# Kernel optimization log

Measured on AMD Instinct MI355X. Metric: run time of the kernel, lower is better.

## Reference

```python
import jax, jax.numpy as jnp
import numpy as np

B, T, H, W, C = 8, 16, 64, 64, 16
HID = 64  # hidden_dim of each ConvLSTM cell
K = 3     # kernel size


def _convlstm_step(x, h, c, Wk, b):
    # conv over concat([x, h]) -> 4*HID gate channels (i, f, o, g)
    z = jax.lax.conv_general_dilated(
        jnp.concatenate([x, h], axis=-1), Wk,
        window_strides=(1, 1), padding='SAME',
        dimension_numbers=('NHWC', 'HWIO', 'NHWC')) + b
    i, f, o, g = jnp.split(z, 4, axis=-1)
    c_new = jax.nn.sigmoid(f) * c + jax.nn.sigmoid(i) * jnp.tanh(g)
    h_new = jax.nn.sigmoid(o) * jnp.tanh(c_new)
    return h_new, c_new


def setup_inputs() -> dict:
    key = jax.random.key(0)
    k1, k2, k3 = jax.random.split(key, 3)
    enc_input = jax.random.normal(k1, (B, T, H, W, C), jnp.float32)
    # input cell: in_channels = C + HID; stacked hidden cell: 2*HID
    W0 = jax.random.normal(k2, (K, K, C + HID, 4 * HID), jnp.float32) * 0.05
    b0 = jnp.zeros((4 * HID,), jnp.float32)
    W1 = jax.random.normal(k3, (K, K, 2 * HID, 4 * HID), jnp.float32) * 0.05
    b1 = jnp.zeros((4 * HID,), jnp.float32)
    return {"enc_input": enc_input, "W0": W0, "b0": b0, "W1": W1, "b1": b1}


def reference(enc_input, W0, b0, W1, b1):
    Bv, Tv, Hv, Wv, _ = enc_input.shape
    z0 = jnp.zeros((Bv, Hv, Wv, HID), enc_input.dtype)

    def step(carry, x_t):
        h0, c0, h1, c1 = carry
        h0, c0 = _convlstm_step(x_t, h0, c0, W0, b0)   # input ConvLSTM
        h1, c1 = _convlstm_step(h0, h1, c1, W1, b1)    # stacked hidden ConvLSTM
        return (h0, c0, h1, c1), None

    xs = jnp.moveaxis(enc_input, 1, 0)  # [T, B, H, W, C]
    (h0, c0, h1, c1), _ = jax.lax.scan(step, (z0, z0, z0, z0), xs)
    # Encoder returns last hidden layer's (h, c)
    return (h1, c1)
```

## Files before the change

### kernel.cpp

```cpp
#include <hip/hip_runtime.h>
#include <hip/hip_bf16.h>

#define Bv 8
#define Tv 16
#define Hv 64
#define Wv 64
#define Cv 16
#define HID 64
#define PH 66

typedef short short8 __attribute__((ext_vector_type(8)));
typedef float f32x4 __attribute__((ext_vector_type(4)));
typedef unsigned short u16x8 __attribute__((ext_vector_type(8)));

__device__ __forceinline__ unsigned short f2bf(float x) {
  union { float f; unsigned int u; } v; v.f = x;
  unsigned int r = v.u + 0x7FFF + ((v.u >> 16) & 1);
  return (unsigned short)(r >> 16);
}
__device__ __forceinline__ float sigmoid_f(float x) {
  return 1.f / (1.f + __expf(-x));
}
__device__ __forceinline__ float tanh_f(float x) {
  float e = __expf(2.f * x);
  return 1.f - 2.f / (e + 1.f);
}

__global__ void relayout_w1(const float* __restrict__ W1, unsigned short* __restrict__ out) {
  int o = blockIdx.x * 256 + threadIdx.x;
  if (o >= 36 * 8192) return;
  int cc = o >> 13, t = o & 8191;
  int wn = t >> 11, t2 = t & 2047;
  int g = t2 >> 9, t3 = t2 & 511;
  int l = t3 >> 3, e = t3 & 7;
  int kg = l >> 4, r = l & 15;
  int k = kg * 8 + e;
  int col = g * 64 + wn * 16 + r;
  int tap = cc >> 2, cgi = cc & 3;
  out[o] = f2bf(W1[(size_t)(tap * 128 + cgi * 32 + k) * 256 + col]);
}

__global__ void relayout_w0(const float* __restrict__ W0, unsigned short* __restrict__ out) {
  int o = blockIdx.x * 256 + threadIdx.x;
  if (o >= 23 * 8192) return;
  int cc = o >> 13, t = o & 8191;
  int wn = t >> 11, t2 = t & 2047;
  int g = t2 >> 9, t3 = t2 & 511;
  int l = t3 >> 3, e = t3 & 7;
  int kg = l >> 4, r = l & 15;
  int k = kg * 8 + e;
  int col = g * 64 + wn * 16 + r;
  float v = 0.f;
  if (cc < 4) {
    int tap = 2 * cc + (k >> 4);
    v = W0[(size_t)(tap * 80 + (k & 15)) * 256 + col];
  } else if (cc == 4) {
    if (k < 16) v = W0[(size_t)(8 * 80 + k) * 256 + col];
  } else {
    int hcc = cc - 5, tap = hcc >> 1, cgi = hcc & 1;
    v = W0[(size_t)(tap * 80 + 16 + cgi * 32 + k) * 256 + col];
  }
  out[o] = f2bf(v);
}

__global__ void zero_init(unsigned short* __restrict__ h0a, unsigned short* __restrict__ h0b,
                          unsigned short* __restrict__ h1a, unsigned short* __restrict__ h1b,
                          unsigned short* __restrict__ xb) {
  int idx = blockIdx.x * 256 + threadIdx.x;
  u16x8 z = {};
  const int XB_CH = (Bv * PH * PH * 16 * 2 * 2) / 16;
  if (idx < XB_CH) { *(u16x8*)(xb + idx * 8) = z; return; }
  idx -= XB_CH;
  int bufi = idx / 16640;
  if (bufi >= 4) return;
  int rem = idx - bufi * 16640;
  int b = rem / 2080, r2 = rem - b * 2080;
  int hp = r2 >> 3, c8 = r2 & 7;
  int y, x;
  if (hp < 66)       { y = 0;  x = hp; }
  else if (hp < 132) { y = 65; x = hp - 66; }
  else { int i2 = hp - 132; y = 1 + (i2 >> 1); x = (i2 & 1) * 65; }
  unsigned short* base = (bufi == 0) ? h0a : (bufi == 1) ? h0b : (bufi == 2) ? h1a : h1b;
  *(u16x8*)(base + ((size_t)((b * PH + y) * PH) + x) * 64 + c8 * 8) = z;
}

__global__ void convert_x0(const float* __restrict__ enc, unsigned short* __restrict__ xb) {
  int idx = blockIdx.x * 256 + threadIdx.x;
  int b = idx >> 12, pix = idx & 4095;
  int y = pix >> 6, x = pix & 63;
  const float* s = enc + ((size_t)(b * Tv + 0) * 4096 + pix) * 16;
  float4 f0 = *(const float4*)(s);
  float4 f1 = *(const float4*)(s + 4);
  float4 f2 = *(const float4*)(s + 8);
  float4 f3 = *(const float4*)(s + 12);
  u16x8 o0, o1;
  o0[0]=f2bf(f0.x); o0[1]=f2bf(f0.y); o0[2]=f2bf(f0.z); o0[3]=f2bf(f0.w);
  o0[4]=f2bf(f1.x); o0[5]=f2bf(f1.y); o0[6]=f2bf(f1.z); o0[7]=f2bf(f1.w);
  o1[0]=f2bf(f2.x); o1[1]=f2bf(f2.y); o1[2]=f2bf(f2.z); o1[3]=f2bf(f2.w);
  o1[4]=f2bf(f3.x); o1[5]=f2bf(f3.y); o1[6]=f2bf(f3.z); o1[7]=f2bf(f3.w);
  unsigned short* d = xb + ((size_t)((b * PH + y + 1) * PH) + (x + 1)) * 16;
  *(u16x8*)(d)     = o0;
  *(u16x8*)(d + 8) = o1;
}

template<int CELL, int NC>
__device__ __forceinline__ void cell_run(
    const char* __restrict__ A0, const char* __restrict__ A1,
    const char* __restrict__ Wr, const float* __restrict__ bias,
    float* __restrict__ cbuf, unsigned short* __restrict__ hout,
    float* __restrict__ h1fin, float* __restrict__ c1fin,
    char* lds, int b, int by, int bx, int tid)
{
  constexpr bool T0C = (CELL == 0) ? (NC == 5) : (NC == 18);
  const int l = tid & 63, w = tid >> 6;
  const int wm = w >> 2, wn = w & 3;
  const int r = l & 15, kg = l >> 4;
  const int j = wn * 16 + r;

  int pixs;
  {
    int ps = w * 16 + r;
    int ys = by * 16 + (ps >> 3), xs = bx * 8 + (ps & 7);
    pixs = (b * PH + ys) * PH + xs;
  }
  const int zpix = b * PH * PH;

  auto ISSUE = [&](int cc, int buf) {
    char* dst = lds + buf * 24576;
    if constexpr (CELL == 0) {
      if (cc < 5) {
        int tapA = 2 * cc;
        int kyA = tapA / 3, kxA = tapA - kyA * 3;
        unsigned offA = (unsigned)((pixs + kyA * PH + kxA) * 32 + kg * 16);
        unsigned offB;
        if (cc < 4) {
          int tapB = tapA + 1;
          int kyB = tapB / 3, kxB = tapB - kyB * 3;
          offB = (unsigned)((pixs + kyB * PH + kxB) * 32 + (kg - 2) * 16);
        } else {
          offB = (unsigned)(zpix * 32 + (kg - 2) * 16);
        }
        unsigned aoff = (kg < 2) ? offA : offB;
        __builtin_amdgcn_global_load_lds((const unsigned int*)(A0 + aoff),
                                         (unsigned int*)(dst + w * 1024), 16, 0, 0);
      } else {
        int hcc = cc - 5, tap = hcc >> 1, cgi = hcc & 1;
        int ky = tap / 3, kx = tap - ky * 3;
        unsigned aoff = (unsigned)((pixs + ky * PH + kx) * 128 + cgi * 64 + kg * 16);
        __builtin_amdgcn_global_load_lds((const unsigned int*)(A1 + aoff),
                                         (unsigned int*)(dst + w * 1024), 16, 0, 0);
      }
    } else {
      int tap, cgi;
      if (T0C) { tap = cc >> 1; cgi = cc & 1; }
      else     { tap = cc >> 2; cgi = cc & 3; }
      int ky = tap / 3, kx = tap - ky * 3;
      const char* srcb = (cgi < 2) ? A0 : A1;
      unsigned aoff = (unsigned)((pixs + ky * PH + kx) * 128 + (cgi & 1) * 64 + kg * 16);
      __builtin_amdgcn_global_load_lds((const unsigned int*)(srcb + aoff),
                                       (unsigned int*)(dst + w * 1024), 16, 0, 0);
    }
    int wcc;
    if constexpr (CELL == 0) wcc = cc;
    else                     wcc = T0C ? ((cc >> 1) * 4 + (cc & 1)) : cc;
    const char* wp = Wr + (size_t)wcc * 16384 + (unsigned)(w * 2048 + l * 16);
    __builtin_amdgcn_global_load_lds((const unsigned int*)(wp),
                                     (unsigned int*)(dst + 8192 + w * 2048), 16, 0, 0);
    __builtin_amdgcn_global_load_lds((const unsigned int*)(wp + 1024),
                                     (unsigned int*)(dst + 8192 + w * 2048 + 1024), 16, 0, 0);
  };

  f32x4 acc[4][4] = {};
  short8 af[4], bfv[4];

  ISSUE(0, 0); ISSUE(1, 1);
#pragma unroll
  for (int cc = 0; cc < NC; ++cc) {
    if (cc <= NC - 2) { asm volatile("s_waitcnt vmcnt(3)" ::: "memory"); }
    else              { asm volatile("s_waitcnt vmcnt(0)" ::: "memory"); }
    __builtin_amdgcn_sched_barrier(0);
    __builtin_amdgcn_s_barrier();
    __builtin_amdgcn_sched_barrier(0);

    if (cc + 2 < NC) ISSUE(cc + 2, (cc + 2) % 3);

    const char* bufp = lds + (cc % 3) * 24576;
#pragma unroll
    for (int mi = 0; mi < 4; ++mi)
      af[mi] = *(const short8*)(bufp + (wm * 4 + mi) * 1024 + l * 16);
#pragma unroll
    for (int g = 0; g < 4; ++g)
      bfv[g] = *(const short8*)(bufp + 8192 + (wn * 4 + g) * 1024 + l * 16);

#pragma unroll
    for (int mi = 0; mi < 4; ++mi)
#pragma unroll
      for (int g = 0; g < 4; ++g)
        acc[mi][g] = __builtin_amdgcn_mfma_f32_16x16x32_bf16(
            af[mi], bfv[g], acc[mi][g], 0, 0, 0);
  }

  float bi[4];
#pragma unroll
  for (int g = 0; g < 4; ++g) bi[g] = bias[g * 64 + j];
  float cpre[4][4];
#pragma unroll
  for (int mi = 0; mi < 4; ++mi) {
#pragma unroll
    for (int rg = 0; rg < 4; ++rg) {
      if constexpr (T0C) { cpre[mi][rg] = 0.f; }
      else {
        int p = wm * 64 + mi * 16 + kg * 4 + rg;
        int y = by * 16 + (p >> 3), x = bx * 8 + (p & 7);
        cpre[mi][rg] = cbuf[((size_t)((b * Hv + y) * Wv) + x) * HID + j];
      }
    }
  }
#pragma unroll
  for (int mi = 0; mi < 4; ++mi) {
#pragma unroll
    for (int rg = 0; rg < 4; ++rg) {
      int p = wm * 64 + mi * 16 + kg * 4 + rg;
      int y = by * 16 + (p >> 3), x = bx * 8 + (p & 7);
      float zi = acc[mi][0][rg] + bi[0];
      float zf = acc[mi][1][rg] + bi[1];
      float zo = acc[mi][2][rg] + bi[2];
      float zg = acc[mi][3][rg] + bi[3];
      float cn = sigmoid_f(zf) * cpre[mi][rg] + sigmoid_f(zi) * tanh_f(zg);
      float hn = sigmoid_f(zo) * tanh_f(cn);
      size_t ci = ((size_t)((b * Hv + y) * Wv) + x) * HID + j;
      cbuf[ci] = cn;
      hout[((size_t)((b * PH + y + 1) * PH) + (x + 1)) * HID + j] = f2bf(hn);
      if (CELL == 1 && h1fin != nullptr) {
        h1fin[ci] = hn;
        c1fin[ci] = cn;
      }
    }
  }
}

template<int NC1, int NC0, bool LAST>
__global__ __launch_bounds__(512, 4)
void step_fused(const unsigned short* __restrict__ xbr, unsigned short* __restrict__ xbw,
                const unsigned short* __restrict__ h0r, unsigned short* __restrict__ h0w,
                const unsigned short* __restrict__ h1r, unsigned short* __restrict__ h1w,
                const unsigned short* __restrict__ w0r, const unsigned short* __restrict__ w1r,
                const float* __restrict__ b0, const float* __restrict__ b1,
                float* __restrict__ c0, float* __restrict__ c1,
                float* __restrict__ h1f, float* __restrict__ c1f,
                const float* __restrict__ enc, int tnext)
{
  extern __shared__ char lds[];
  const int tid = threadIdx.x;
  const int gid = blockIdx.x;
  int isC1, k;
  if constexpr (NC1 > 0 && NC0 > 0) { isC1 = gid & 1; k = gid >> 1; }
  else if constexpr (NC1 > 0)       { isC1 = 1; k = gid; }
  else                              { isC1 = 0; k = gid; }
  const int b = k >> 5, rem = k & 31;
  const int by = rem >> 3, bx = rem & 7;

  if constexpr (NC1 > 0) {
    if (isC1) {
      cell_run<1, NC1>((const char*)h0r, (const char*)h1r, (const char*)w1r, b1,
                       c1, h1w, LAST ? h1f : nullptr, LAST ? c1f : nullptr,
                       lds, b, by, bx, tid);
      return;
    }
  }
  if constexpr (NC0 > 0) {
    cell_run<0, NC0>((const char*)xbr, (const char*)h0r, (const char*)w0r, b0,
                     c0, h0w, nullptr, nullptr, lds, b, by, bx, tid);
    if (tnext >= 0) {
      int pp = tid >> 2, q4 = tid & 3;
      int y = by * 16 + (pp >> 3), x = bx * 8 + (pp & 7);
      const float* s = enc + ((size_t)(b * Tv + tnext) * 4096 + (y * 64 + x)) * 16 + q4 * 4;
      float4 f = *(const float4*)s;
      unsigned short* d = xbw + ((size_t)((b * PH + y + 1) * PH) + (x + 1)) * 16 + q4 * 4;
      d[0] = f2bf(f.x); d[1] = f2bf(f.y); d[2] = f2bf(f.z); d[3] = f2bf(f.w);
    }
  }
}

extern "C" void kernel_launch(void* const* d_in, const int* in_sizes, int n_in,
                              void* d_out, int out_size, void* d_ws, size_t ws_size,
                              hipStream_t stream) {
  const float* enc = (const float*)d_in[0];
  const float* W0  = (const float*)d_in[1];
  const float* b0  = (const float*)d_in[2];
  const float* W1  = (const float*)d_in[3];
  const float* b1  = (const float*)d_in[4];

  float* out = (float*)d_out;
  const size_t NST = (size_t)Bv * Hv * Wv * HID;
  float* h1f = out;
  float* c1  = out + NST;

  char* ws = (char*)d_ws;
  const size_t SZ_C = NST * 4;
  const size_t SZ_H = (size_t)Bv * PH * PH * HID * 2;
  const size_t SZ_X = (size_t)Bv * PH * PH * 16 * 2;
  float*          c0  = (float*)ws;
  unsigned short* h0a = (unsigned short*)(ws + SZ_C);
  unsigned short* h0b = (unsigned short*)(ws + SZ_C + SZ_H);
  unsigned short* h1a = (unsigned short*)(ws + SZ_C + 2 * SZ_H);
  unsigned short* h1b = (unsigned short*)(ws + SZ_C + 3 * SZ_H);
  unsigned short* xb0 = (unsigned short*)(ws + SZ_C + 4 * SZ_H);
  unsigned short* xb1 = (unsigned short*)(ws + SZ_C + 4 * SZ_H + SZ_X);
  unsigned short* w0r = (unsigned short*)(ws + SZ_C + 4 * SZ_H + 2 * SZ_X);
  unsigned short* w1r = (unsigned short*)(ws + SZ_C + 4 * SZ_H + 2 * SZ_X + (size_t)23 * 16384);

  hipFuncSetAttribute((const void*)step_fused<0,5,false>,   hipFuncAttributeMaxDynamicSharedMemorySize, 73728);
  hipFuncSetAttribute((const void*)step_fused<18,23,false>, hipFuncAttributeMaxDynamicSharedMemorySize, 73728);
  hipFuncSetAttribute((const void*)step_fused<36,23,false>, hipFuncAttributeMaxDynamicSharedMemorySize, 73728);
  hipFuncSetAttribute((const void*)step_fused<36,0,true>,   hipFuncAttributeMaxDynamicSharedMemorySize, 73728);

  zero_init<<<805, 256, 0, stream>>>(h0a, h0b, h1a, h1b, xb0);
  relayout_w0<<<736, 256, 0, stream>>>(W0, w0r);
  relayout_w1<<<1152, 256, 0, stream>>>(W1, w1r);
  convert_x0<<<128, 256, 0, stream>>>(enc, xb0);

  const int LDSB = 73728;
  step_fused<0,5,false><<<256, 512, LDSB, stream>>>(
      xb0, xb1, h0b, h0a, h1a, h1b, w0r, w1r, b0, b1, c0, c1,
      nullptr, nullptr, enc, 1);
  for (int t = 1; t <= 15; ++t) {
    unsigned short* h0r = (t & 1) ? h0a : h0b;
    unsigned short* h0w = (t & 1) ? h0b : h0a;
    unsigned short* h1r = (t & 1) ? h1b : h1a;
    unsigned short* h1w = (t & 1) ? h1a : h1b;
    unsigned short* xr  = (t & 1) ? xb1 : xb0;
    unsigned short* xw  = (t & 1) ? xb0 : xb1;
    int tn = (t + 1 <= 15) ? (t + 1) : -1;
    if (t == 1)
      step_fused<18,23,false><<<512, 512, LDSB, stream>>>(
          xr, xw, h0r, h0w, h1r, h1w, w0r, w1r, b0, b1, c0, c1,
          nullptr, nullptr, enc, tn);
    else
      step_fused<36,23,false><<<512, 512, LDSB, stream>>>(
          xr, xw, h0r, h0w, h1r, h1w, w0r, w1r, b0, b1, c0, c1,
          nullptr, nullptr, enc, tn);
  }
  step_fused<36,0,true><<<256, 512, LDSB, stream>>>(
      xb0, xb1, h0b, h0a, h1a, h1b, w0r, w1r, b0, b1, c0, c1,
      h1f, c1, enc, -1);
}
```

Baseline: 649.1 us.

## Load activation fragments directly to registers and deepen weight LDS pipeline to four stages

Activation (A) fragments are now read straight from global memory into registers one chunk ahead, instead of being staged through LDS. Only the weight (B) tiles still go through LDS, now as a 4-buffer ring that prefetches three chunks ahead, with vmcnt waits recomputed to match. The W1 relayout is reordered so all h0-source chunks come before the h1-source chunks, which simplifies the chunk-to-source mapping. This cuts LDS traffic and footprint (from 72KB to 64KB). The risk is that A reads are now uncoalesced per-wave global loads whose latency must be hidden behind the MFMAs, and they use more registers.

```diff
diff --git a/kernel.cpp b/kernel.cpp
--- a/kernel.cpp
+++ b/kernel.cpp
@@ -36,8 +36,10 @@
   int kg = l >> 4, r = l & 15;
   int k = kg * 8 + e;
   int col = g * 64 + wn * 16 + r;
-  int tap = cc >> 2, cgi = cc & 3;
-  out[o] = f2bf(W1[(size_t)(tap * 128 + cgi * 32 + k) * 256 + col]);
+  int row;
+  if (cc < 18) { int tap = cc >> 1; row = tap * 128 + (cc & 1) * 32 + k; }
+  else { int h = cc - 18; int tap = h >> 1; row = tap * 128 + 64 + (h & 1) * 32 + k; }
+  out[o] = f2bf(W1[(size_t)row * 256 + col]);
 }
 
 __global__ void relayout_w0(const float* __restrict__ W0, unsigned short* __restrict__ out) {
@@ -117,80 +119,91 @@
   const int r = l & 15, kg = l >> 4;
   const int j = wn * 16 + r;
 
-  int pixs;
+  int pix0;
   {
-    int ps = w * 16 + r;
-    int ys = by * 16 + (ps >> 3), xs = bx * 8 + (ps & 7);
-    pixs = (b * PH + ys) * PH + xs;
+    int p = wm * 64 + r;
+    int y = by * 16 + (p >> 3), x = bx * 8 + (p & 7);
+    pix0 = (b * PH + y) * PH + x;
   }
   const int zpix = b * PH * PH;
 
   auto ISSUE = [&](int cc, int buf) {
-    char* dst = lds + buf * 24576;
+    char* dst = lds + buf * 16384;
+    const char* wp = Wr + (size_t)cc * 16384 + (unsigned)(w * 2048 + l * 16);
+    __builtin_amdgcn_global_load_lds((const unsigned int*)wp,
+                                     (unsigned int*)(dst + w * 2048), 16, 0, 0);
+    __builtin_amdgcn_global_load_lds((const unsigned int*)(wp + 1024),
+                                     (unsigned int*)(dst + w * 2048 + 1024), 16, 0, 0);
+  };
+
+  short8 af[4], bfv[4];
+
+  auto LOADA = [&](int cc) {
     if constexpr (CELL == 0) {
       if (cc < 5) {
-        int tapA = 2 * cc;
-        int kyA = tapA / 3, kxA = tapA - kyA * 3;
-        unsigned offA = (unsigned)((pixs + kyA * PH + kxA) * 32 + kg * 16);
-        unsigned offB;
-        if (cc < 4) {
-          int tapB = tapA + 1;
-          int kyB = tapB / 3, kxB = tapB - kyB * 3;
-          offB = (unsigned)((pixs + kyB * PH + kxB) * 32 + (kg - 2) * 16);
-        } else {
-          offB = (unsigned)(zpix * 32 + (kg - 2) * 16);
+        int tapA = 2 * cc, kyA = tapA / 3, kxA = tapA - kyA * 3;
+#pragma unroll
+        for (int mi = 0; mi < 4; ++mi) {
+          int pm = pix0 + mi * (2 * PH);
+          unsigned offA = (unsigned)((pm + kyA * PH + kxA) * 32 + kg * 16);
+          unsigned offB;
+          if (cc < 4) {
+            int tapB = 2 * cc + 1, kyB = tapB / 3, kxB = tapB - kyB * 3;
+            offB = (unsigned)((pm + kyB * PH + kxB) * 32 + (kg - 2) * 16);
+          } else {
+            offB = (unsigned)(zpix * 32 + (kg - 2) * 16);
+          }
+          af[mi] = *(const short8*)(A0 + ((kg < 2) ? offA : offB));
         }
-        unsigned aoff = (kg < 2) ? offA : offB;
-        __builtin_amdgcn_global_load_lds((const unsigned int*)(A0 + aoff),
-                                         (unsigned int*)(dst + w * 1024), 16, 0, 0);
       } else {
         int hcc = cc - 5, tap = hcc >> 1, cgi = hcc & 1;
         int ky = tap / 3, kx = tap - ky * 3;
-        unsigned aoff = (unsigned)((pixs + ky * PH + kx) * 128 + cgi * 64 + kg * 16);
-        __builtin_amdgcn_global_load_lds((const unsigned int*)(A1 + aoff),
-                                         (unsigned int*)(dst + w * 1024), 16, 0, 0);
+#pragma unroll
+        for (int mi = 0; mi < 4; ++mi) {
+          int pm = pix0 + mi * (2 * PH);
+          af[mi] = *(const short8*)(A1 + (unsigned)((pm + ky * PH + kx) * 128 + cgi * 64 + kg * 16));
+        }
       }
     } else {
-      int tap, cgi;
-      if (T0C) { tap = cc >> 1; cgi = cc & 1; }
-      else     { tap = cc >> 2; cgi = cc & 3; }
+      const char* srcb; int tap, half;
+      if (cc < 18) { tap = cc >> 1; half = cc & 1; srcb = A0; }
+      else         { int h = cc - 18; tap = h >> 1; half = h & 1; srcb = A1; }
       int ky = tap / 3, kx = tap - ky * 3;
-      const char* srcb = (cgi < 2) ? A0 : A1;
-      unsigned aoff = (unsigned)((pixs + ky * PH + kx) * 128 + (cgi & 1) * 64 + kg * 16);
-      __builtin_amdgcn_global_load_lds((const unsigned int*)(srcb + aoff),
-                                       (unsigned int*)(dst + w * 1024), 16, 0, 0);
-    }
-    int wcc;
-    if constexpr (CELL == 0) wcc = cc;
-    else                     wcc = T0C ? ((cc >> 1) * 4 + (cc & 1)) : cc;
-    const char* wp = Wr + (size_t)wcc * 16384 + (unsigned)(w * 2048 + l * 16);
-    __builtin_amdgcn_global_load_lds((const unsigned int*)(wp),
-                                     (unsigned int*)(dst + 8192 + w * 2048), 16, 0, 0);
-    __builtin_amdgcn_global_load_lds((const unsigned int*)(wp + 1024),
-                                     (unsigned int*)(dst + 8192 + w * 2048 + 1024), 16, 0, 0);
+#pragma unroll
+      for (int mi = 0; mi < 4; ++mi) {
+        int pm = pix0 + mi * (2 * PH);
+        af[mi] = *(const short8*)(srcb + (unsigned)((pm + ky * PH + kx) * 128 + half * 64 + kg * 16));
+      }
+    }
   };
 
   f32x4 acc[4][4] = {};
-  short8 af[4], bfv[4];
-
-  ISSUE(0, 0); ISSUE(1, 1);
+
+  ISSUE(0, 0); ISSUE(1, 1); ISSUE(2, 2);
+  __builtin_amdgcn_sched_barrier(0);
+  LOADA(0);
+  __builtin_amdgcn_sched_barrier(0);
+
 #pragma unroll
   for (int cc = 0; cc < NC; ++cc) {
-    if (cc <= NC - 2) { asm volatile("s_waitcnt vmcnt(3)" ::: "memory"); }
-    else              { asm volatile("s_waitcnt vmcnt(0)" ::: "memory"); }
+    {
+      const int N = (cc == 0) ? 8 : (cc == 1) ? 12
+                  : 12 + ((cc + 1 < NC) ? 2 : 0) + ((cc + 2 < NC) ? 2 : 0);
+      if      (N == 8)  asm volatile("s_waitcnt vmcnt(8)"  ::: "memory");
+      else if (N == 12) asm volatile("s_waitcnt vmcnt(12)" ::: "memory");
+      else if (N == 14) asm volatile("s_waitcnt vmcnt(14)" ::: "memory");
+      else              asm volatile("s_waitcnt vmcnt(16)" ::: "memory");
+    }
     __builtin_amdgcn_sched_barrier(0);
     __builtin_amdgcn_s_barrier();
     __builtin_amdgcn_sched_barrier(0);
 
-    if (cc + 2 < NC) ISSUE(cc + 2, (cc + 2) % 3);
-
-    const char* bufp = lds + (cc % 3) * 24576;
-#pragma unroll
-    for (int mi = 0; mi < 4; ++mi)
-      af[mi] = *(const short8*)(bufp + (wm * 4 + mi) * 1024 + l * 16);
+    const char* bufp = lds + (cc & 3) * 16384;
 #pragma unroll
     for (int g = 0; g < 4; ++g)
-      bfv[g] = *(const short8*)(bufp + 8192 + (wn * 4 + g) * 1024 + l * 16);
+      bfv[g] = *(const short8*)(bufp + (wn * 4 + g) * 1024 + l * 16);
+    if (cc + 3 < NC) ISSUE(cc + 3, (cc + 3) & 3);
+    __builtin_amdgcn_sched_barrier(0);
 
 #pragma unroll
     for (int mi = 0; mi < 4; ++mi)
@@ -198,6 +211,8 @@
       for (int g = 0; g < 4; ++g)
         acc[mi][g] = __builtin_amdgcn_mfma_f32_16x16x32_bf16(
             af[mi], bfv[g], acc[mi][g], 0, 0, 0);
+    if (cc + 1 < NC) LOADA(cc + 1);
+    __builtin_amdgcn_sched_barrier(0);
   }
 
   float bi[4];
@@ -310,17 +325,17 @@
   unsigned short* w0r = (unsigned short*)(ws + SZ_C + 4 * SZ_H + 2 * SZ_X);
   unsigned short* w1r = (unsigned short*)(ws + SZ_C + 4 * SZ_H + 2 * SZ_X + (size_t)23 * 16384);
 
-  hipFuncSetAttribute((const void*)step_fused<0,5,false>,   hipFuncAttributeMaxDynamicSharedMemorySize, 73728);
-  hipFuncSetAttribute((const void*)step_fused<18,23,false>, hipFuncAttributeMaxDynamicSharedMemorySize, 73728);
-  hipFuncSetAttribute((const void*)step_fused<36,23,false>, hipFuncAttributeMaxDynamicSharedMemorySize, 73728);
-  hipFuncSetAttribute((const void*)step_fused<36,0,true>,   hipFuncAttributeMaxDynamicSharedMemorySize, 73728);
+  hipFuncSetAttribute((const void*)step_fused<0,5,false>,   hipFuncAttributeMaxDynamicSharedMemorySize, 65536);
+  hipFuncSetAttribute((const void*)step_fused<18,23,false>, hipFuncAttributeMaxDynamicSharedMemorySize, 65536);
+  hipFuncSetAttribute((const void*)step_fused<36,23,false>, hipFuncAttributeMaxDynamicSharedMemorySize, 65536);
+  hipFuncSetAttribute((const void*)step_fused<36,0,true>,   hipFuncAttributeMaxDynamicSharedMemorySize, 65536);
 
   zero_init<<<805, 256, 0, stream>>>(h0a, h0b, h1a, h1b, xb0);
   relayout_w0<<<736, 256, 0, stream>>>(W0, w0r);
   relayout_w1<<<1152, 256, 0, stream>>>(W1, w1r);
   convert_x0<<<128, 256, 0, stream>>>(enc, xb0);
 
-  const int LDSB = 73728;
+  const int LDSB = 65536;
   step_fused<0,5,false><<<256, 512, LDSB, stream>>>(
       xb0, xb1, h0b, h0a, h1a, h1b, w0r, w1r, b0, b1, c0, c1,
       nullptr, nullptr, enc, 1);
```

New measurement: 1.327 ms. 104% more time.
